# Kernel tuning notes

Measured on AMD Instinct MI355X. Metric: run time of the kernel, lower is better.

The kernel has to match this reference:

```python
import jax, jax.numpy as jnp
import numpy as np

N = 128                      # reduced state dimension (Q_dim[0])
S = N * (N + 1) // 2         # number of triu pairwise products = 8256
BATCH = 16384                # snapshot columns
_rows, _cols = np.triu_indices(N)
ROWS = jnp.asarray(_rows)    # [S] int32 constants
COLS = jnp.asarray(_cols)


def setup_inputs() -> dict:
    key = jax.random.key(0)
    kx, ka, kb = jax.random.split(key, 3)
    x = jax.random.normal(kx, (N, BATCH), dtype=jnp.float32)
    # learned operators (module inits them to zeros; use small random for a meaningful baseline)
    A = jax.random.normal(ka, (N, N), dtype=jnp.float32) * 0.02
    B = jax.random.normal(kb, (N, S), dtype=jnp.float32) * 0.02
    return {"x": x, "A": A, "B": B}


def reference(x, A, B):
    # quadratic feature expansion: x2[k, :] = x[i_k, :] * x[j_k, :] over triu pairs
    x2 = x[ROWS] * x[COLS]                 # [S, BATCH]
    return A @ x + B @ x2                  # [N, BATCH]
```

## Files before the change

kernel.cpp:

```cpp
#include <hip/hip_runtime.h>


constexpr int N_     = 128;
constexpr int S_     = 8256;
constexpr int BATCH_ = 16384;
constexpr int KTOT   = 8384;
constexpr int NKT    = 131;
constexpr size_t WT_BYTES = (size_t)KTOT * 128 * 2;
constexpr size_t PP_OFF   = WT_BYTES;

typedef __attribute__((ext_vector_type(8))) _Float16 half8;
typedef __attribute__((ext_vector_type(2))) _Float16 half2t;
typedef __attribute__((ext_vector_type(4))) float f32x4;

__device__ __forceinline__ ushort f2h(float f) {
    _Float16 h = (_Float16)f;
    ushort b; __builtin_memcpy(&b, &h, 2); return b;
}
__device__ __forceinline__ float h2f(ushort b) {
    _Float16 h; __builtin_memcpy(&h, &b, 2); return (float)h;
}
__device__ __forceinline__ half2t duph(ushort b) {
    uint w = ((uint)b << 16) | (uint)b;
    half2t d; __builtin_memcpy(&d, &w, 4); return d;
}
__device__ __forceinline__ half8 mul_bc(half8 w, half2t d) {
    union { half8 h; half2t p[4]; } u, r;
    u.h = w;
    #pragma unroll
    for (int q = 0; q < 4; ++q) r.p[q] = u.p[q] * d;
    return r.h;
}

__device__ __forceinline__ int cumN(int i) {
    if (i <= 0) return 0;
    const int n = i - 1, t = n >> 3, r = n & 7;
    return 16 * i - (4 * t * (t + 1) + r * (t + 1));
}
__device__ __forceinline__ int offR(int i) {
    const int a = i >> 3, b = i & 7;
    const int p = b ? (8 * (b - 1) - (((b - 1) * b) >> 1)) : 0;
    return 28 * a + p;
}
__device__ __forceinline__ int triS(int i) { return i * (257 - i) / 2; }

__global__ __launch_bounds__(256) void build_all(
    const float* __restrict__ A, const float* __restrict__ B,
    ushort* __restrict__ pp, ushort* __restrict__ wt,
    float* __restrict__ out)
{
    const int bid = blockIdx.x, t = threadIdx.x;
    if (bid < 524) {
        const int idx = bid * 256 + t;
        const int ko  = idx >> 7;
        const int m   = idx & 127;
        const int kt = ko >> 3, kk = (ko >> 2) & 1, oct = ko & 3;
        const int lane = oct * 16 + (m & 15);
        const int e0 = kt * 8192 + kk * 4096 + (m >> 6) * 2048 +
                       ((m >> 4) & 3) * 512 + lane * 8;
        float v[8];
        if (ko < 16) {
            const int i0 = ko * 8;
            #pragma unroll
            for (int el = 0; el < 8; ++el) v[el] = A[m * 128 + i0 + el];
        } else if (ko < 992) {
            const int o = ko - 16;
            int i = 0;
            #pragma unroll
            for (int st = 64; st >= 1; st >>= 1) {
                const int c = i + st;
                if (c < 128 && cumN(c) <= o) i = c;
            }
            const int jb = ((i + 7) >> 3) + (o - cumN(i));
            const int s0 = triS(i) + jb * 8 - i;
            const float* bp = B + (size_t)m * S_ + s0;
            #pragma unroll
            for (int el = 0; el < 8; ++el) v[el] = bp[el];
        } else {
            const int kb = ko * 8 - 7936;
            #pragma unroll
            for (int el = 0; el < 8; ++el) {
                const int kloc = kb + el;
                int i = 0;
                #pragma unroll
                for (int st = 64; st >= 1; st >>= 1) {
                    const int c = i + st;
                    if (c < 128 && offR(c) <= kloc) i = c;
                }
                v[el] = B[(size_t)m * S_ + triS(i) + (kloc - offR(i))];
            }
        }
        ushort o8[8];
        #pragma unroll
        for (int el = 0; el < 8; ++el) o8[el] = f2h(v[el]);
        __builtin_memcpy(wt + e0, o8, 16);
    } else if (bid < 780) {
        const int zb = bid - 524;
        f32x4* o4 = (f32x4*)out;
        #pragma unroll
        for (int c = 0; c < 4; ++c)
            o4[(size_t)zb * 2048 + c * 512 + t] = (f32x4){0.f, 0.f, 0.f, 0.f};
    } else {
        const int i = t;
        if (i < 128) {
            pp[i] = (ushort)(i | (0xFFu << 8));
            const int jb0 = (i + 7) >> 3;
            int kb = 128 + cumN(i) * 8;
            for (int jb = jb0; jb < 16; ++jb) {
                #pragma unroll
                for (int e = 0; e < 8; ++e)
                    pp[kb + e] = (ushort)(i | ((jb * 8 + e) << 8));
                kb += 8;
            }
            const int h = (8 - (i & 7)) & 7;
            const int rb = 7936 + offR(i);
            for (int e = 0; e < h; ++e)
                pp[rb + e] = (ushort)(i | ((i + e) << 8));
        }
    }
}

__device__ __forceinline__ void load_af(half8 af[8], const ushort* __restrict__ wt,
                                        int kt, int wm, int lane) {
    const ushort* ab = wt + ((size_t)kt << 13) + (wm << 11) + (lane << 3);
    #pragma unroll
    for (int kk = 0; kk < 2; ++kk)
        #pragma unroll
        for (int mt = 0; mt < 4; ++mt)
            af[kk * 4 + mt] = *(const half8*)(ab + (kk << 12) + (mt << 9));
}

__device__ __forceinline__ void step_nice(f32x4 acc[4][4], const half8 af[8],
                                          uint w0, uint w1,
                                          const ushort* __restrict__ xbase,
                                          int sw) {
    const int ia = (int)(w0 & 0xFFu) ^ sw, ja = (int)((w0 >> 8) & 0xFFu) ^ sw;
    const int ib = (int)(w1 & 0xFFu) ^ sw, jb = (int)((w1 >> 8) & 0xFFu) ^ sw;
    ushort xi[2][4];
    half8  wj[2][4];
    #pragma unroll
    for (int nt = 0; nt < 4; ++nt) {
        const ushort* xb = xbase + nt * 2048;
        xi[0][nt] = xb[ia];
        xi[1][nt] = xb[ib];
        wj[0][nt] = *(const half8*)(xb + ja);
        wj[1][nt] = *(const half8*)(xb + jb);
    }
    #pragma unroll
    for (int kk = 0; kk < 2; ++kk)
        #pragma unroll
        for (int nt = 0; nt < 4; ++nt) {
            const half8 bfr = mul_bc(wj[kk][nt], duph(xi[kk][nt]));
            #pragma unroll
            for (int mt = 0; mt < 4; ++mt)
                acc[mt][nt] = __builtin_amdgcn_mfma_f32_16x16x32_f16(
                    af[kk * 4 + mt], bfr, acc[mt][nt], 0, 0, 0);
        }
}

__global__ __launch_bounds__(512) void gemm_mfma(
    const float*  __restrict__ x,
    const ushort* __restrict__ wt,
    const ushort* __restrict__ pp,
    float* __restrict__ out)
{
    __shared__ ushort xt[256 * 128];

    const int t    = threadIdx.x;
    const int b0   = blockIdx.x * 256;
    const int sp   = blockIdx.y;
    const int kt0  = sp * 33;
    const int kt1  = (sp == 3) ? NKT : kt0 + 33;
    const int lane = t & 63;
    const int w    = t >> 6;
    const int wm   = w >> 2, wn = w & 3;
    const int l16  = lane & 15, quad = lane >> 4;
    const int sw   = (l16 & 7) << 3;

    {
        const int n = t & 255, g = t >> 8;
        const int swn = (n & 7) << 3;
        #pragma unroll
        for (int c = 0; c < 8; ++c) {
            const int rb = g * 64 + c * 8;
            uint ow[4];
            #pragma unroll
            for (int p = 0; p < 4; ++p) {
                const ushort u0 = f2h(x[(size_t)(rb + 2 * p) * BATCH_ + b0 + n]);
                const ushort u1 = f2h(x[(size_t)(rb + 2 * p + 1) * BATCH_ + b0 + n]);
                ow[p] = (uint)u0 | ((uint)u1 << 16);
            }
            __builtin_memcpy(&xt[n * 128 + (rb ^ swn)], ow, 16);
        }
    }
    __syncthreads();

    f32x4 acc[4][4];
    #pragma unroll
    for (int mt = 0; mt < 4; ++mt)
        #pragma unroll
        for (int nt = 0; nt < 4; ++nt)
            acc[mt][nt] = (f32x4){0.f, 0.f, 0.f, 0.f};

    const ushort* xbase = xt + (wn * 64 + l16) * 128;

    if (sp == 0) {
        for (int kt = 0; kt < 2; ++kt) {
            half8 af[8];
            load_af(af, wt, kt, wm, lane);
            #pragma unroll
            for (int kk = 0; kk < 2; ++kk) {
                const int off = (kt * 64 + kk * 32 + quad * 8) ^ sw;
                #pragma unroll
                for (int nt = 0; nt < 4; ++nt) {
                    const half8 bfr = *(const half8*)(xbase + nt * 2048 + off);
                    #pragma unroll
                    for (int mt = 0; mt < 4; ++mt)
                        acc[mt][nt] = __builtin_amdgcn_mfma_f32_16x16x32_f16(
                            af[kk * 4 + mt], bfr, acc[mt][nt], 0, 0, 0);
                }
            }
        }
    }

    {
        const int s_ni = (kt0 > 2) ? kt0 : 2;
        const int e_ni = (kt1 < 124) ? kt1 : 124;
        int kt = s_ni;
        if (kt < e_ni) {
            half8 afA[8], afB[8];
            load_af(afA, wt, kt, wm, lane);
            uint w0 = *(const uint*)(pp + kt * 64 + quad * 8);
            uint w1 = *(const uint*)(pp + kt * 64 + 32 + quad * 8);
            while (true) {
                {
                    const int ktn = (kt + 1 < e_ni) ? kt + 1 : kt;
                    load_af(afB, wt, ktn, wm, lane);
                    const uint nw0 = *(const uint*)(pp + ktn * 64 + quad * 8);
                    const uint nw1 = *(const uint*)(pp + ktn * 64 + 32 + quad * 8);
                    step_nice(acc, afA, w0, w1, xbase, sw);
                    w0 = nw0; w1 = nw1; ++kt;
                }
                if (kt >= e_ni) break;
                {
                    const int ktn = (kt + 1 < e_ni) ? kt + 1 : kt;
                    load_af(afA, wt, ktn, wm, lane);
                    const uint nw0 = *(const uint*)(pp + ktn * 64 + quad * 8);
                    const uint nw1 = *(const uint*)(pp + ktn * 64 + 32 + quad * 8);
                    step_nice(acc, afB, w0, w1, xbase, sw);
                    w0 = nw0; w1 = nw1; ++kt;
                }
                if (kt >= e_ni) break;
            }
        }
    }

    if (sp == 3) {
        for (int kt = 124; kt < NKT; ++kt) {
            half8 af[8];
            load_af(af, wt, kt, wm, lane);
            #pragma unroll
            for (int kk = 0; kk < 2; ++kk) {
                const int k0 = kt * 64 + kk * 32 + quad * 8;
                const uint4 pk = *(const uint4*)(pp + k0);
                const uint pr4[4] = {pk.x, pk.y, pk.z, pk.w};
                #pragma unroll
                for (int nt = 0; nt < 4; ++nt) {
                    const ushort* xb = xbase + nt * 2048;
                    float prods[8];
                    #pragma unroll
                    for (int e = 0; e < 8; ++e) {
                        const uint ent = (pr4[e >> 1] >> ((e & 1) * 16)) & 0xFFFFu;
                        prods[e] = h2f(xb[(int)(ent & 0xFFu) ^ sw]) *
                                   h2f(xb[(int)(ent >> 8) ^ sw]);
                    }
                    union { half8 h; uint wdw[4]; } bb;
                    #pragma unroll
                    for (int p = 0; p < 4; ++p) {
                        const auto pk2 = __builtin_amdgcn_cvt_pkrtz(
                            prods[2 * p], prods[2 * p + 1]);
                        __builtin_memcpy(&bb.wdw[p], &pk2, 4);
                    }
                    const half8 bfr = bb.h;
                    #pragma unroll
                    for (int mt = 0; mt < 4; ++mt)
                        acc[mt][nt] = __builtin_amdgcn_mfma_f32_16x16x32_f16(
                            af[kk * 4 + mt], bfr, acc[mt][nt], 0, 0, 0);
                }
            }
        }
    }

    #pragma unroll
    for (int mt = 0; mt < 4; ++mt) {
        #pragma unroll
        for (int nt = 0; nt < 4; ++nt) {
            const int mbase = wm * 64 + mt * 16 + quad * 4;
            const size_t col = (size_t)b0 + wn * 64 + nt * 16 + l16;
            #pragma unroll
            for (int r = 0; r < 4; ++r)
                unsafeAtomicAdd(&out[(size_t)(mbase + r) * BATCH_ + col],
                                acc[mt][nt][r]);
        }
    }
}

extern "C" void kernel_launch(void* const* d_in, const int* in_sizes, int n_in,
                              void* d_out, int out_size, void* d_ws, size_t ws_size,
                              hipStream_t stream) {
    const float* x = (const float*)d_in[0];
    const float* A = (const float*)d_in[1];
    const float* B = (const float*)d_in[2];
    float* out = (float*)d_out;

    ushort* wt = (ushort*)d_ws;
    ushort* pp = (ushort*)((char*)d_ws + PP_OFF);

    build_all<<<781, 256, 0, stream>>>(A, B, pp, wt, out);
    gemm_mfma<<<dim3(BATCH_ / 256, 4), 512, 0, stream>>>(x, wt, pp, out);
}
```

Measured before the change: 128.4 us.

## Software-pipeline LDS gathers ahead of MFMAs and stagger wave start tiles

Splits the triangular K-step into a shared-memory gather phase and an MFMA phase, so the gathers for the next k-tile are issued before the MFMAs for the current one. The MFMA burst is wrapped in s_setprio to favour matrix issue. Each of the eight waves also starts at a different offset within its k-range and wraps around, which spreads global weight reads and LDS bank traffic across waves. This costs extra registers for the double-buffered gather fragments and may lower occupancy or cause spills.

```diff
diff --git a/kernel.cpp b/kernel.cpp
--- a/kernel.cpp
+++ b/kernel.cpp
@@ -130,14 +130,12 @@
             af[kk * 4 + mt] = *(const half8*)(ab + (kk << 12) + (mt << 9));
 }
 
-__device__ __forceinline__ void step_nice(f32x4 acc[4][4], const half8 af[8],
-                                          uint w0, uint w1,
-                                          const ushort* __restrict__ xbase,
-                                          int sw) {
+__device__ __forceinline__ void read_bin(ushort xi[2][4], half8 wj[2][4],
+                                         uint w0, uint w1,
+                                         const ushort* __restrict__ xbase,
+                                         int sw) {
     const int ia = (int)(w0 & 0xFFu) ^ sw, ja = (int)((w0 >> 8) & 0xFFu) ^ sw;
     const int ib = (int)(w1 & 0xFFu) ^ sw, jb = (int)((w1 >> 8) & 0xFFu) ^ sw;
-    ushort xi[2][4];
-    half8  wj[2][4];
     #pragma unroll
     for (int nt = 0; nt < 4; ++nt) {
         const ushort* xb = xbase + nt * 2048;
@@ -146,16 +144,27 @@
         wj[0][nt] = *(const half8*)(xb + ja);
         wj[1][nt] = *(const half8*)(xb + jb);
     }
+}
+
+__device__ __forceinline__ void mfma_step(f32x4 acc[4][4], const half8 af[8],
+                                          const ushort xi[2][4],
+                                          const half8 wj[2][4]) {
+    half8 bfr[2][4];
     #pragma unroll
     for (int kk = 0; kk < 2; ++kk)
         #pragma unroll
-        for (int nt = 0; nt < 4; ++nt) {
-            const half8 bfr = mul_bc(wj[kk][nt], duph(xi[kk][nt]));
+        for (int nt = 0; nt < 4; ++nt)
+            bfr[kk][nt] = mul_bc(wj[kk][nt], duph(xi[kk][nt]));
+    __builtin_amdgcn_s_setprio(1);
+    #pragma unroll
+    for (int kk = 0; kk < 2; ++kk)
+        #pragma unroll
+        for (int nt = 0; nt < 4; ++nt)
             #pragma unroll
             for (int mt = 0; mt < 4; ++mt)
                 acc[mt][nt] = __builtin_amdgcn_mfma_f32_16x16x32_f16(
-                    af[kk * 4 + mt], bfr, acc[mt][nt], 0, 0, 0);
-        }
+                    af[kk * 4 + mt], bfr[kk][nt], acc[mt][nt], 0, 0, 0);
+    __builtin_amdgcn_s_setprio(0);
 }
 
 __global__ __launch_bounds__(512) void gemm_mfma(
@@ -226,31 +235,44 @@
     {
         const int s_ni = (kt0 > 2) ? kt0 : 2;
         const int e_ni = (kt1 < 124) ? kt1 : 124;
-        int kt = s_ni;
-        if (kt < e_ni) {
-            half8 afA[8], afB[8];
+        const int len  = e_ni - s_ni;
+        if (len > 0) {
+            int kt  = s_ni + ((w * len) >> 3);
+            int ktn = (kt + 1 < e_ni) ? kt + 1 : s_ni;
+
+            half8  afA[8], afB[8];
+            ushort xiA[2][4], xiB[2][4];
+            half8  wjA[2][4], wjB[2][4];
+
+            const uint c0 = *(const uint*)(pp + kt * 64 + quad * 8);
+            const uint c1 = *(const uint*)(pp + kt * 64 + 32 + quad * 8);
             load_af(afA, wt, kt, wm, lane);
-            uint w0 = *(const uint*)(pp + kt * 64 + quad * 8);
-            uint w1 = *(const uint*)(pp + kt * 64 + 32 + quad * 8);
+            uint n0 = *(const uint*)(pp + ktn * 64 + quad * 8);
+            uint n1 = *(const uint*)(pp + ktn * 64 + 32 + quad * 8);
+            read_bin(xiA, wjA, c0, c1, xbase, sw);
+
+            int rem = len;
             while (true) {
                 {
-                    const int ktn = (kt + 1 < e_ni) ? kt + 1 : kt;
+                    const int kt2 = (ktn + 1 < e_ni) ? ktn + 1 : s_ni;
+                    const uint m0 = *(const uint*)(pp + kt2 * 64 + quad * 8);
+                    const uint m1 = *(const uint*)(pp + kt2 * 64 + 32 + quad * 8);
                     load_af(afB, wt, ktn, wm, lane);
-                    const uint nw0 = *(const uint*)(pp + ktn * 64 + quad * 8);
-                    const uint nw1 = *(const uint*)(pp + ktn * 64 + 32 + quad * 8);
-                    step_nice(acc, afA, w0, w1, xbase, sw);
-                    w0 = nw0; w1 = nw1; ++kt;
-                }
-                if (kt >= e_ni) break;
+                    read_bin(xiB, wjB, n0, n1, xbase, sw);
+                    mfma_step(acc, afA, xiA, wjA);
+                    n0 = m0; n1 = m1; ktn = kt2;
+                    if (--rem == 0) break;
+                }
                 {
-                    const int ktn = (kt + 1 < e_ni) ? kt + 1 : kt;
+                    const int kt2 = (ktn + 1 < e_ni) ? ktn + 1 : s_ni;
+                    const uint m0 = *(const uint*)(pp + kt2 * 64 + quad * 8);
+                    const uint m1 = *(const uint*)(pp + kt2 * 64 + 32 + quad * 8);
                     load_af(afA, wt, ktn, wm, lane);
-                    const uint nw0 = *(const uint*)(pp + ktn * 64 + quad * 8);
-                    const uint nw1 = *(const uint*)(pp + ktn * 64 + 32 + quad * 8);
-                    step_nice(acc, afB, w0, w1, xbase, sw);
-                    w0 = nw0; w1 = nw1; ++kt;
-                }
-                if (kt >= e_ni) break;
+                    read_bin(xiA, wjA, n0, n1, xbase, sw);
+                    mfma_step(acc, afB, xiB, wjB);
+                    n0 = m0; n1 = m1; ktn = kt2;
+                    if (--rem == 0) break;
+                }
             }
         }
     }
```

Measured after the change: 119.6 us. -6.8%, faster.
